# Optimization experiments

Measured on AMD Instinct MI355X. Metric: run time of the kernel, lower is better.

The kernel has to match this reference:

```python
import jax, jax.numpy as jnp
import numpy as np

LORA_SCALING = 1.0 / 4.0  # lora_alpha / lora_rank
NUM_HEADS = 16
HEAD_DIM = 64
ROPE_BASE = 20000.0


def rotate_half(x):
    x1, x2 = jnp.split(x, 2, axis=-1)
    return jnp.concatenate([-x2, x1], axis=-1)


def setup_inputs() -> dict:
    key = jax.random.key(0)
    ks = jax.random.split(key, 8)
    B, S, D = 8, 1024, 1024
    hidden_states = jax.random.normal(ks[0], (B, S, D), jnp.float32)
    attention_mask = jnp.zeros((B, 1, 1, S), jnp.float32)
    # real rotary tables (HF style: duplicated half-dim freqs)
    inv_freq = 1.0 / (ROPE_BASE ** (jnp.arange(0, HEAD_DIM, 2, dtype=jnp.float32) / HEAD_DIM))
    t = jnp.arange(S, dtype=jnp.float32)
    freqs = jnp.outer(t, inv_freq)                      # [S, hd/2]
    emb = jnp.concatenate([freqs, freqs], axis=-1)      # [S, hd]
    cos = jnp.broadcast_to(jnp.cos(emb)[None], (B, S, HEAD_DIM))
    sin = jnp.broadcast_to(jnp.sin(emb)[None], (B, S, HEAD_DIM))
    adapter_mask = jax.random.randint(ks[1], (B,), 0, 5, jnp.int32)
    Wqkv_weight = jax.random.normal(ks[2], (3 * D, D), jnp.float32) * 0.02
    Wqkv_bias = jax.random.normal(ks[3], (3 * D,), jnp.float32) * 0.02
    lora_A = jax.random.normal(ks[4], (5, 4, D), jnp.float32) * 0.02
    lora_B = jax.random.normal(ks[5], (5, 3 * D, 4), jnp.float32) * 0.02
    return dict(hidden_states=hidden_states, attention_mask=attention_mask,
                cos=cos, sin=sin, adapter_mask=adapter_mask,
                Wqkv_weight=Wqkv_weight, Wqkv_bias=Wqkv_bias,
                lora_A=lora_A, lora_B=lora_B)


def reference(hidden_states, attention_mask, cos, sin, adapter_mask,
              Wqkv_weight, Wqkv_bias, lora_A, lora_B):
    B, S, D = hidden_states.shape
    H, hd = NUM_HEADS, HEAD_DIM
    # fused QKV projection with per-task LoRA (gather adapters per batch row)
    base = jnp.einsum('bsd,od->bso', hidden_states, Wqkv_weight) + Wqkv_bias
    A_t = lora_A[adapter_mask]                    # [B, r, D]
    B_t = lora_B[adapter_mask]                    # [B, 3D, r]
    lo = jnp.einsum('bsd,brd->bsr', hidden_states, A_t)
    delta = jnp.einsum('bsr,bor->bso', lo, B_t) * LORA_SCALING
    qkv = (base + delta).reshape(B, S, 3, H, hd)
    q = qkv[:, :, 0].transpose(0, 2, 1, 3)        # [B,H,S,hd]
    k = qkv[:, :, 1].transpose(0, 2, 1, 3)
    v = qkv[:, :, 2].transpose(0, 2, 1, 3)
    # inline RoPE
    c = cos[:, None, :, :]
    s = sin[:, None, :, :]
    q = q * c + rotate_half(q) * s
    k = k * c + rotate_half(k) * s
    # eager SDPA
    scaling = hd ** -0.5
    scores = jnp.einsum('bhqd,bhkd->bhqk', q, k) * scaling + attention_mask
    attn = jax.nn.softmax(scores, axis=-1)
    out = jnp.einsum('bhqk,bhkd->bhqd', attn, v)
    return out.transpose(0, 2, 1, 3).reshape(B, S, H * hd)
```

## Files before the change

kernel.cpp:

```cpp
#include <hip/hip_runtime.h>
#include <hip/hip_bf16.h>
#include <stdint.h>

typedef __attribute__((ext_vector_type(8))) short short8;
typedef __attribute__((ext_vector_type(4))) float f32x4;
typedef unsigned short ushort_t;

#define MFMA16(a, b, c) __builtin_amdgcn_mfma_f32_16x16x32_bf16((a), (b), (c), 0, 0, 0)
#define EXP2F(x) __builtin_amdgcn_exp2f(x)
#define BAR() __builtin_amdgcn_s_barrier()


__device__ __forceinline__ float bf2f(unsigned short u) {
    union { unsigned int i; float f; } x; x.i = ((unsigned int)u) << 16; return x.f;
}
__device__ __forceinline__ unsigned short f2bf(float f) {
    union { float f; unsigned int i; } x; x.f = f;
    unsigned int i = x.i;
    i = i + 0x7FFFu + ((i >> 16) & 1u);
    return (unsigned short)(i >> 16);
}
__device__ __forceinline__ unsigned int pack2(float a, float b) {
    return (unsigned int)f2bf(a) | ((unsigned int)f2bf(b) << 16);
}
__device__ __forceinline__ void glds16(const void* gsrc, void* ldst) {
    __builtin_amdgcn_global_load_lds(
        (const __attribute__((address_space(1))) unsigned int*)gsrc,
        (__attribute__((address_space(3))) unsigned int*)ldst, 16, 0, 0);
}

__global__ __launch_bounds__(256) void prep_kernel(
    const float* __restrict__ hidden,
    const float* __restrict__ W,
    const float* __restrict__ loraA,
    const int* __restrict__ adapter_mask,
    ushort_t* __restrict__ Hb,
    ushort_t* __restrict__ Wb,
    float4* __restrict__ lo)
{
    int tid = threadIdx.x;
    int wave = tid >> 6, lane = tid & 63;
    int row = blockIdx.x * 4 + wave;
    if (row < 8192) {
        int b = row >> 10;
        int a = adapter_mask[b];
        const float4* hp = (const float4*)(hidden + (size_t)row * 1024);
        float4 hv[4];
#pragma unroll
        for (int c = 0; c < 4; ++c) hv[c] = hp[c * 64 + lane];
#pragma unroll
        for (int c = 0; c < 4; ++c) {
            uint2 pk;
            pk.x = pack2(hv[c].x, hv[c].y);
            pk.y = pack2(hv[c].z, hv[c].w);
            *(uint2*)(Hb + (size_t)row * 1024 + c * 256 + lane * 4) = pk;
        }
        const float4* Ap = (const float4*)(loraA + (size_t)a * 4096);
        float acc[4];
#pragma unroll
        for (int r = 0; r < 4; ++r) {
            float s = 0.f;
#pragma unroll
            for (int c = 0; c < 4; ++c) {
                float4 av = Ap[(size_t)r * 256 + c * 64 + lane];
                s += hv[c].x * av.x + hv[c].y * av.y + hv[c].z * av.z + hv[c].w * av.w;
            }
            acc[r] = s;
        }
        for (int off = 32; off > 0; off >>= 1)
#pragma unroll
            for (int r = 0; r < 4; ++r) acc[r] += __shfl_xor(acc[r], off);
        if (lane == 0) lo[row] = make_float4(acc[0], acc[1], acc[2], acc[3]);
    } else {
        int rw = row - 8192;
        const float4* wp = (const float4*)(W + (size_t)rw * 1024);
        float4 wv[4];
#pragma unroll
        for (int c = 0; c < 4; ++c) wv[c] = wp[c * 64 + lane];
#pragma unroll
        for (int c = 0; c < 4; ++c) {
            uint2 pk;
            pk.x = pack2(wv[c].x, wv[c].y);
            pk.y = pack2(wv[c].z, wv[c].w);
            *(uint2*)(Wb + (size_t)rw * 1024 + c * 256 + lane * 4) = pk;
        }
    }
}

__global__ __launch_bounds__(256, 4) void qkv_gemm_kernel(
    const ushort_t* __restrict__ Hb,
    const ushort_t* __restrict__ Wb,
    const float* __restrict__ bias,
    const float4* __restrict__ lo,
    const float* __restrict__ loraB,
    const int* __restrict__ adapter_mask,
    const float* __restrict__ cosp,
    const float* __restrict__ sinp,
    ushort_t* __restrict__ qw,
    ushort_t* __restrict__ kw,
    ushort_t* __restrict__ vt)
{
    __shared__ __align__(16) ushort_t As[2][4096];
    __shared__ __align__(16) ushort_t Bs[2][4096];
    int tid = threadIdx.x;
    int wave = tid >> 6, lane = tid & 63, quad = lane >> 4, l16 = lane & 15;
    int mq = (wave >> 1) * 64, nq = (wave & 1) * 64;

    int wg = (blockIdx.x & 7) * 192 + (blockIdx.x >> 3);
    int bx = wg % 24, by = wg / 24;
    int n0 = bx * 128;
    int m0 = by * 128;

    int r_ = tid >> 2;
    int c_ = (tid & 3) ^ ((tid >> 3) & 3);
    const ushort_t* pA0 = Hb + (size_t)(m0 + r_) * 1024 + c_ * 8;
    const ushort_t* pA1 = pA0 + (size_t)64 * 1024;
    const ushort_t* pB0 = Wb + (size_t)(n0 + r_) * 1024 + c_ * 8;
    const ushort_t* pB1 = pB0 + (size_t)64 * 1024;
    char* dA = (char*)&As[0][0] + wave * 1024;
    char* dB = (char*)&Bs[0][0] + wave * 1024;

    int offA[4], offB[4];
#pragma unroll
    for (int i = 0; i < 4; ++i) {
        int ra = mq + i * 16 + l16;
        offA[i] = ra * 64 + ((quad ^ ((ra >> 1) & 3)) * 16);
        int rb = nq + i * 16 + l16;
        offB[i] = rb * 64 + ((quad ^ ((rb >> 1) & 3)) * 16);
    }

    f32x4 acc[4][4];
#pragma unroll
    for (int i = 0; i < 4; ++i)
#pragma unroll
        for (int j = 0; j < 4; ++j) acc[i][j] = (f32x4)0.f;

    glds16(pA0, dA);  glds16(pA1, dA + 4096);
    glds16(pB0, dB);  glds16(pB1, dB + 4096);
    __syncthreads();

#pragma unroll 2
    for (int t = 0; t < 32; ++t) {
        int cur = t & 1;
        if (t < 31) {
            int k = (t + 1) * 32;
            char* sA = dA + (cur ^ 1) * 8192;
            char* sB = dB + (cur ^ 1) * 8192;
            glds16(pA0 + k, sA);  glds16(pA1 + k, sA + 4096);
            glds16(pB0 + k, sB);  glds16(pB1 + k, sB + 4096);
        }
        const char* rA = (const char*)&As[0][0] + cur * 8192;
        const char* rB = (const char*)&Bs[0][0] + cur * 8192;
        short8 af[4], bf[4];
#pragma unroll
        for (int i = 0; i < 4; ++i) af[i] = *(const short8*)(rA + offA[i]);
#pragma unroll
        for (int i = 0; i < 4; ++i) bf[i] = *(const short8*)(rB + offB[i]);
#pragma unroll
        for (int mi = 0; mi < 4; ++mi)
#pragma unroll
            for (int ni = 0; ni < 4; ++ni)
                acc[mi][ni] = MFMA16(af[mi], bf[ni], acc[mi][ni]);
        __syncthreads();
    }

    int t_qkv = n0 >> 10;
    int b = m0 >> 10;
    int a_idx = adapter_mask[b];
    float bi[4], bb[4][4];
    int cpos[4], chh[4];
#pragma unroll
    for (int ni = 0; ni < 4; ++ni) {
        int c = n0 + nq + ni * 16 + l16;
        bi[ni] = bias[c];
        const float* Bp = loraB + ((size_t)a_idx * 3072 + c) * 4;
        bb[ni][0] = Bp[0]; bb[ni][1] = Bp[1]; bb[ni][2] = Bp[2]; bb[ni][3] = Bp[3];
        cpos[ni] = c & 63; chh[ni] = (c >> 6) & 15;
    }
#pragma unroll
    for (int mi = 0; mi < 4; ++mi) {
        float vals[4][4];
#pragma unroll
        for (int r = 0; r < 4; ++r) {
            int m = m0 + mq + mi * 16 + quad * 4 + r;
            float4 lov = lo[m];
#pragma unroll
            for (int ni = 0; ni < 4; ++ni)
                vals[r][ni] = acc[mi][ni][r] + bi[ni]
                      + 0.25f * (lov.x * bb[ni][0] + lov.y * bb[ni][1]
                               + lov.z * bb[ni][2] + lov.w * bb[ni][3]);
        }
        int s0 = (m0 + mq + mi * 16 + quad * 4) & 1023;
        if (t_qkv < 2) {
#pragma unroll
            for (int r = 0; r < 4; ++r) {
                int s = s0 + r;
                size_t cb = ((size_t)b * 1024 + s) * 64;
                float cA = cosp[cb + l16],      sA_ = sinp[cb + l16];
                float cB = cosp[cb + 16 + l16], sB_ = sinp[cb + 16 + l16];
                float w0 = vals[r][0] * cA - vals[r][2] * sA_;
                float w2 = vals[r][2] * cA + vals[r][0] * sA_;
                float w1 = vals[r][1] * cB - vals[r][3] * sB_;
                float w3 = vals[r][3] * cB + vals[r][1] * sB_;
                float v[4] = {w0, w1, w2, w3};
#pragma unroll
                for (int ni = 0; ni < 4; ++ni) {
                    size_t bh = (size_t)b * 16 + chh[ni];
                    ushort_t ob = f2bf(v[ni]);
                    if (t_qkv == 0) qw[(bh * 1024 + s) * 64 + cpos[ni]] = ob;
                    else            kw[(bh * 1024 + s) * 64 + cpos[ni]] = ob;
                }
            }
        } else {
#pragma unroll
            for (int ni = 0; ni < 4; ++ni) {
                uint2 pk;
                pk.x = pack2(vals[0][ni], vals[1][ni]);
                pk.y = pack2(vals[2][ni], vals[3][ni]);
                size_t bh = (size_t)b * 16 + chh[ni];
                *(uint2*)&vt[(bh * 64 + cpos[ni]) * 1024 + s0] = pk;
            }
        }
    }
}

__global__ __launch_bounds__(256, 2) void attn_kernel(
    const ushort_t* __restrict__ qw,
    const ushort_t* __restrict__ kw,
    const ushort_t* __restrict__ vt,
    const float* __restrict__ mask,
    float* __restrict__ out)
{
    __shared__ __align__(16) ushort_t Kt[3][4096];
    __shared__ __align__(16) ushort_t Vt[3][4096];
    __shared__ __align__(16) ushort_t Ps[4][32][72];
    __shared__ float mlds[1024];
    const float KSCALE = 0.125f * 1.44269504f;
    int tid = threadIdx.x;
    int wave = tid >> 6, lane = tid & 63, quad = lane >> 4, l16 = lane & 15;
    int id = blockIdx.x;
    int qp = id >> 7;
    int bh = id & 127;
    int b = bh >> 4, h = bh & 15;
    size_t base = (size_t)bh * 65536;
    int q0 = qp * 256 + wave * 32;

    for (int i = tid; i < 1024; i += 256) mlds[i] = mask[b * 1024 + i] * 1.44269504f;

    const ushort_t* kbase = kw + base;
    const ushort_t* vbase = vt + base;

    int n0 = tid, n1 = tid + 256;
    int r0 = n0 >> 3, c0 = (n0 & 7) ^ (r0 & 7);
    int r1 = n1 >> 3, c1 = (n1 & 7) ^ (r1 & 7);

    short8 qf[4][2];
    for (int mt = 0; mt < 4; ++mt) {
        int qr = q0 + (mt >> 1) * 128 + (mt & 1) * 16;
        for (int kt = 0; kt < 2; ++kt)
            qf[mt][kt] = *(const short8*)(qw + base + (size_t)(qr + l16) * 64 + kt * 32 + quad * 8);
    }

    f32x4 oacc[4][4], sum_acc[4];
    for (int mt = 0; mt < 4; ++mt) {
        sum_acc[mt] = (f32x4)0.f;
        for (int nt = 0; nt < 4; ++nt) oacc[mt][nt] = (f32x4)0.f;
    }

    short8 ones;
    for (int j = 0; j < 8; ++j) ones[j] = (short)0x3F80;

    __syncthreads();

    int koff[4][2], voff[4][2];
    for (int nt = 0; nt < 4; ++nt)
        for (int kt = 0; kt < 2; ++kt) {
            int rr = nt * 16 + l16;
            int cc = (kt * 4 + quad) ^ (rr & 7);
            koff[nt][kt] = (rr * 8 + cc) * 8;
            voff[nt][kt] = (rr * 8 + cc) * 8;
        }

    {
        char* kd = (char*)&Kt[0][0] + wave * 1024;
        char* vd = (char*)&Vt[0][0] + wave * 1024;
        glds16(kbase + (size_t)r0 * 64 + c0 * 8, kd);
        glds16(kbase + (size_t)r1 * 64 + c1 * 8, kd + 4096);
        glds16(vbase + (size_t)r0 * 1024 + c0 * 8, vd);
        glds16(vbase + (size_t)r1 * 1024 + c1 * 8, vd + 4096);
        kd = (char*)&Kt[1][0] + wave * 1024;
        vd = (char*)&Vt[1][0] + wave * 1024;
        glds16(kbase + (size_t)(64 + r0) * 64 + c0 * 8, kd);
        glds16(kbase + (size_t)(64 + r1) * 64 + c1 * 8, kd + 4096);
        glds16(vbase + (size_t)r0 * 1024 + 64 + c0 * 8, vd);
        glds16(vbase + (size_t)r1 * 1024 + 64 + c1 * 8, vd + 4096);
    }

    const ushort_t* kR  = &Kt[0][0];  const ushort_t* vR  = &Vt[0][0];
    const ushort_t* kN1 = &Kt[1][0];  const ushort_t* vN1 = &Vt[1][0];
    const ushort_t* kN2 = &Kt[2][0];  const ushort_t* vN2 = &Vt[2][0];

    for (int it = 0; it < 16; ++it) {
        int kt0 = it * 64;
        if (it < 15) { asm volatile("s_waitcnt vmcnt(4)" ::: "memory"); }
        else         { asm volatile("s_waitcnt vmcnt(0)" ::: "memory"); }
        BAR();
        __builtin_amdgcn_sched_barrier(0);
        if (it < 14) {
            int kn = kt0 + 128;
            char* kd = (char*)kN2 + wave * 1024;
            char* vd = (char*)vN2 + wave * 1024;
            glds16(kbase + (size_t)(kn + r0) * 64 + c0 * 8, kd);
            glds16(kbase + (size_t)(kn + r1) * 64 + c1 * 8, kd + 4096);
            glds16(vbase + (size_t)r0 * 1024 + kn + c0 * 8, vd);
            glds16(vbase + (size_t)r1 * 1024 + kn + c1 * 8, vd + 4096);
        }
        float mv[4];
        for (int nt = 0; nt < 4; ++nt) mv[nt] = mlds[kt0 + nt * 16 + l16];

#pragma unroll
        for (int ph = 0; ph < 2; ++ph) {
            f32x4 sacc[2][4];
            {
                short8 kf[4][2];
#pragma unroll
                for (int nt = 0; nt < 4; ++nt)
#pragma unroll
                    for (int kt = 0; kt < 2; ++kt)
                        kf[nt][kt] = *(const short8*)&kR[koff[nt][kt]];
#pragma unroll
                for (int mt = 0; mt < 2; ++mt)
#pragma unroll
                    for (int nt = 0; nt < 4; ++nt) {
                        f32x4 z = (f32x4)0.f;
                        z = MFMA16(qf[ph * 2 + mt][0], kf[nt][0], z);
                        z = MFMA16(qf[ph * 2 + mt][1], kf[nt][1], z);
                        sacc[mt][nt] = z;
                    }
            }
#pragma unroll
            for (int mt = 0; mt < 2; ++mt)
#pragma unroll
                for (int nt = 0; nt < 4; ++nt)
#pragma unroll
                    for (int r = 0; r < 4; ++r) {
                        float p = EXP2F(sacc[mt][nt][r] * KSCALE + mv[nt]);
                        Ps[wave][mt * 16 + quad * 4 + r][nt * 16 + l16] = f2bf(p);
                    }
            short8 pf[2][2];
#pragma unroll
            for (int mt = 0; mt < 2; ++mt)
#pragma unroll
                for (int kt = 0; kt < 2; ++kt)
                    pf[mt][kt] = *(const short8*)&Ps[wave][mt * 16 + l16][kt * 32 + quad * 8];
            {
                short8 vf[4][2];
#pragma unroll
                for (int nt = 0; nt < 4; ++nt)
#pragma unroll
                    for (int kt = 0; kt < 2; ++kt)
                        vf[nt][kt] = *(const short8*)&vR[voff[nt][kt]];
#pragma unroll
                for (int mt = 0; mt < 2; ++mt) {
#pragma unroll
                    for (int nt = 0; nt < 4; ++nt) {
                        oacc[ph * 2 + mt][nt] = MFMA16(pf[mt][0], vf[nt][0], oacc[ph * 2 + mt][nt]);
                        oacc[ph * 2 + mt][nt] = MFMA16(pf[mt][1], vf[nt][1], oacc[ph * 2 + mt][nt]);
                    }
                    sum_acc[ph * 2 + mt] = MFMA16(pf[mt][0], ones, sum_acc[ph * 2 + mt]);
                    sum_acc[ph * 2 + mt] = MFMA16(pf[mt][1], ones, sum_acc[ph * 2 + mt]);
                }
            }
        }
        const ushort_t* tk = kR; kR = kN1; kN1 = kN2; kN2 = tk;
        const ushort_t* tv = vR; vR = vN1; vN1 = vN2; vN2 = tv;
    }

    for (int mt = 0; mt < 4; ++mt) {
        for (int r = 0; r < 4; ++r) {
            float inv = 1.f / sum_acc[mt][r];
            int s = q0 + (mt >> 1) * 128 + (mt & 1) * 16 + quad * 4 + r;
            size_t ob = ((size_t)b * 1024 + s) * 1024 + h * 64;
            for (int nt = 0; nt < 4; ++nt)
                out[ob + nt * 16 + l16] = oacc[mt][nt][r] * inv;
        }
    }
}

extern "C" void kernel_launch(void* const* d_in, const int* in_sizes, int n_in,
                              void* d_out, int out_size, void* d_ws, size_t ws_size,
                              hipStream_t stream)
{
    const float* hidden = (const float*)d_in[0];
    const float* mask   = (const float*)d_in[1];
    const float* cosp   = (const float*)d_in[2];
    const float* sinp   = (const float*)d_in[3];
    const int* adapter_mask = (const int*)d_in[4];
    const float* W      = (const float*)d_in[5];
    const float* bias   = (const float*)d_in[6];
    const float* loraA  = (const float*)d_in[7];
    const float* loraB  = (const float*)d_in[8];
    float* out = (float*)d_out;

    char* ws = (char*)d_ws;
    float4* lo = (float4*)ws;
    ushort_t* qw = (ushort_t*)(ws + (1 << 20));
    ushort_t* kw = qw + (size_t)8 * 16 * 1024 * 64;
    ushort_t* vt = kw + (size_t)8 * 16 * 1024 * 64;

    ushort_t* Hb = (ushort_t*)d_out;
    ushort_t* Wb = Hb + (size_t)8192 * 1024;

    prep_kernel<<<2816, 256, 0, stream>>>(hidden, W, loraA, adapter_mask, Hb, Wb, lo);
    qkv_gemm_kernel<<<1536, 256, 0, stream>>>(Hb, Wb, bias, lo, loraB, adapter_mask,
                                              cosp, sinp, qw, kw, vt);
    attn_kernel<<<512, 256, 0, stream>>>(qw, kw, vt, mask, out);
}
```

Baseline: 238.1 us.

## Triple-buffer QKV GEMM LDS staging with single barrier and vmcnt waits

Moves the QKV GEMM main loop from double to triple LDS buffering, prefetching two k-steps ahead. The per-iteration __syncthreads is replaced by an explicit s_waitcnt vmcnt plus one barrier at the top, and buffer pointers rotate each step. This hides more global-load latency, but the larger LDS footprint drops the occupancy hint from 4 to 3 blocks per CU. Correctness now depends on the hand-written vmcnt counts matching the number of outstanding loads.

```diff
diff --git a/kernel.cpp b/kernel.cpp
--- a/kernel.cpp
+++ b/kernel.cpp
@@ -9,6 +9,7 @@
 #define MFMA16(a, b, c) __builtin_amdgcn_mfma_f32_16x16x32_bf16((a), (b), (c), 0, 0, 0)
 #define EXP2F(x) __builtin_amdgcn_exp2f(x)
 #define BAR() __builtin_amdgcn_s_barrier()
+#define CFENCE() asm volatile("" ::: "memory")
 
 
 __device__ __forceinline__ float bf2f(unsigned short u) {
@@ -87,7 +88,7 @@
     }
 }
 
-__global__ __launch_bounds__(256, 4) void qkv_gemm_kernel(
+__global__ __launch_bounds__(256, 3) void qkv_gemm_kernel(
     const ushort_t* __restrict__ Hb,
     const ushort_t* __restrict__ Wb,
     const float* __restrict__ bias,
@@ -100,8 +101,8 @@
     ushort_t* __restrict__ kw,
     ushort_t* __restrict__ vt)
 {
-    __shared__ __align__(16) ushort_t As[2][4096];
-    __shared__ __align__(16) ushort_t Bs[2][4096];
+    __shared__ __align__(16) ushort_t As[3][4096];
+    __shared__ __align__(16) ushort_t Bs[3][4096];
     int tid = threadIdx.x;
     int wave = tid >> 6, lane = tid & 63, quad = lane >> 4, l16 = lane & 15;
     int mq = (wave >> 1) * 64, nq = (wave & 1) * 64;
@@ -117,8 +118,7 @@
     const ushort_t* pA1 = pA0 + (size_t)64 * 1024;
     const ushort_t* pB0 = Wb + (size_t)(n0 + r_) * 1024 + c_ * 8;
     const ushort_t* pB1 = pB0 + (size_t)64 * 1024;
-    char* dA = (char*)&As[0][0] + wave * 1024;
-    char* dB = (char*)&Bs[0][0] + wave * 1024;
+    int woff = wave * 1024;
 
     int offA[4], offB[4];
 #pragma unroll
@@ -135,33 +135,37 @@
 #pragma unroll
         for (int j = 0; j < 4; ++j) acc[i][j] = (f32x4)0.f;
 
-    glds16(pA0, dA);  glds16(pA1, dA + 4096);
-    glds16(pB0, dB);  glds16(pB1, dB + 4096);
-    __syncthreads();
-
-#pragma unroll 2
+    char* bA_r  = (char*)&As[0][0];  char* bB_r  = (char*)&Bs[0][0];
+    char* bA_n1 = (char*)&As[1][0];  char* bB_n1 = (char*)&Bs[1][0];
+    char* bA_n2 = (char*)&As[2][0];  char* bB_n2 = (char*)&Bs[2][0];
+
+    glds16(pA0,      bA_r  + woff);  glds16(pA1,      bA_r  + woff + 4096);
+    glds16(pB0,      bB_r  + woff);  glds16(pB1,      bB_r  + woff + 4096);
+    glds16(pA0 + 32, bA_n1 + woff);  glds16(pA1 + 32, bA_n1 + woff + 4096);
+    glds16(pB0 + 32, bB_n1 + woff);  glds16(pB1 + 32, bB_n1 + woff + 4096);
+
     for (int t = 0; t < 32; ++t) {
-        int cur = t & 1;
-        if (t < 31) {
-            int k = (t + 1) * 32;
-            char* sA = dA + (cur ^ 1) * 8192;
-            char* sB = dB + (cur ^ 1) * 8192;
-            glds16(pA0 + k, sA);  glds16(pA1 + k, sA + 4096);
-            glds16(pB0 + k, sB);  glds16(pB1 + k, sB + 4096);
-        }
-        const char* rA = (const char*)&As[0][0] + cur * 8192;
-        const char* rB = (const char*)&Bs[0][0] + cur * 8192;
+        if (t < 31) { asm volatile("s_waitcnt vmcnt(4)" ::: "memory"); }
+        else        { asm volatile("s_waitcnt vmcnt(0)" ::: "memory"); }
+        BAR();
+        CFENCE();
+        if (t < 30) {
+            int k = (t + 2) * 32;
+            glds16(pA0 + k, bA_n2 + woff);  glds16(pA1 + k, bA_n2 + woff + 4096);
+            glds16(pB0 + k, bB_n2 + woff);  glds16(pB1 + k, bB_n2 + woff + 4096);
+        }
         short8 af[4], bf[4];
 #pragma unroll
-        for (int i = 0; i < 4; ++i) af[i] = *(const short8*)(rA + offA[i]);
-#pragma unroll
-        for (int i = 0; i < 4; ++i) bf[i] = *(const short8*)(rB + offB[i]);
+        for (int i = 0; i < 4; ++i) af[i] = *(const short8*)(bA_r + offA[i]);
+#pragma unroll
+        for (int i = 0; i < 4; ++i) bf[i] = *(const short8*)(bB_r + offB[i]);
 #pragma unroll
         for (int mi = 0; mi < 4; ++mi)
 #pragma unroll
             for (int ni = 0; ni < 4; ++ni)
                 acc[mi][ni] = MFMA16(af[mi], bf[ni], acc[mi][ni]);
-        __syncthreads();
+        char* tA = bA_r; bA_r = bA_n1; bA_n1 = bA_n2; bA_n2 = tA;
+        char* tB = bB_r; bB_r = bB_n1; bB_n1 = bB_n2; bB_n2 = tB;
     }
 
     int t_qkv = n0 >> 10;
```

Measured after the change: 228.3 us. -4.1%, faster.
